# Kernel tuning notes

Measured on AMD Instinct MI355X. Metric: run time of the kernel, lower is better.

## Reference

```python
import jax, jax.numpy as jnp
import numpy as np

H = 768
FF = 3072
NH = 12
DH = H // NH


def setup_inputs() -> dict:
    key = jax.random.key(0)
    ks = jax.random.split(key, 16)
    s = 0.02
    return {
        "latent": jax.random.normal(ks[0], (2, 2048, H), jnp.float32),
        "ln1_w": jnp.ones((H,), jnp.float32),
        "ln1_b": jnp.zeros((H,), jnp.float32),
        "Wq": jax.random.normal(ks[1], (H, H), jnp.float32) * s,
        "bq": jnp.zeros((H,), jnp.float32),
        "Wk": jax.random.normal(ks[2], (H, H), jnp.float32) * s,
        "bk": jnp.zeros((H,), jnp.float32),
        "Wv": jax.random.normal(ks[3], (H, H), jnp.float32) * s,
        "bv": jnp.zeros((H,), jnp.float32),
        "Wo": jax.random.normal(ks[4], (H, H), jnp.float32) * s,
        "bo": jnp.zeros((H,), jnp.float32),
        "ln2_w": jnp.ones((H,), jnp.float32),
        "ln2_b": jnp.zeros((H,), jnp.float32),
        "W1": jax.random.normal(ks[5], (H, FF), jnp.float32) * s,
        "b1": jnp.zeros((FF,), jnp.float32),
        "W2": jax.random.normal(ks[6], (FF, H), jnp.float32) * s,
        "b2": jnp.zeros((H,), jnp.float32),
    }


def _layernorm(x, w, b, eps=1e-6):
    mu = jnp.mean(x, axis=-1, keepdims=True)
    var = jnp.mean(jnp.square(x - mu), axis=-1, keepdims=True)
    return (x - mu) * jax.lax.rsqrt(var + eps) * w + b


def _split_heads(x):  # [B,S,H] -> [B,NH,S,DH]
    B, S, _ = x.shape
    return x.reshape(B, S, NH, DH).transpose(0, 2, 1, 3)


def reference(latent, ln1_w, ln1_b, Wq, bq, Wk, bk, Wv, bv, Wo, bo,
              ln2_w, ln2_b, W1, b1, W2, b2):
    B, S, _ = latent.shape
    # MHSA (dropouts are p=0.0 / eval mode -> identity)
    nx = _layernorm(latent, ln1_w, ln1_b)
    q = _split_heads(nx @ Wq + bq)
    k = _split_heads(nx @ Wk + bk)
    v = _split_heads(nx @ Wv + bv)
    scores = jnp.einsum('bhqd,bhkd->bhqk', q, k) / jnp.sqrt(jnp.float32(DH))
    attn = jax.nn.softmax(scores, axis=-1)
    ctx = jnp.einsum('bhqk,bhkd->bhqd', attn, v)
    ctx = ctx.transpose(0, 2, 1, 3).reshape(B, S, H)
    latent = latent + (ctx @ Wo + bo)
    # FFN (exact erf GELU as in torch nn.GELU default)
    nx = _layernorm(latent, ln2_w, ln2_b)
    h = jax.nn.gelu(nx @ W1 + b1, approximate=False)
    latent = latent + (h @ W2 + b2)
    return latent
```

## Files before the change

kernel.cpp:

```cpp
#include <hip/hip_runtime.h>

#define H 768
#define FF 3072
#define NH 12
#define DH 64
#define SEQ 2048
#define MTOK 4096

typedef __attribute__((ext_vector_type(8))) short short8;
typedef __attribute__((ext_vector_type(4))) float f32x4;
typedef __attribute__((ext_vector_type(2))) unsigned int uint2v;

__device__ __forceinline__ f32x4 mfma16(short8 a, short8 b, f32x4 c) {
  return __builtin_amdgcn_mfma_f32_16x16x32_bf16(a, b, c, 0, 0, 0);
}

__device__ __forceinline__ unsigned short f2bf(float f) {
  union { float f; unsigned int u; } c; c.f = f;
  unsigned int u = c.u;
  u += 0x7fffu + ((u >> 16) & 1u);
  return (unsigned short)(u >> 16);
}
__device__ __forceinline__ float bf2f(unsigned short s) {
  union { unsigned int u; float f; } c; c.u = ((unsigned int)s) << 16;
  return c.f;
}
__device__ __forceinline__ unsigned int pk2bf(float lo, float hi) {
  return (unsigned int)f2bf(lo) | ((unsigned int)f2bf(hi) << 16);
}
__device__ __forceinline__ unsigned int pktrunc(float lo, float hi) {
  union { float f; unsigned int u; } a, b; a.f = hi; b.f = lo;
  return __builtin_amdgcn_perm(a.u, b.u, 0x07060302u);
}

__device__ __forceinline__ void gld16(const unsigned short* g, unsigned short* l) {
  __builtin_amdgcn_global_load_lds(
      (const __attribute__((address_space(1))) void*)g,
      (__attribute__((address_space(3))) void*)l, 16, 0, 0);
}

__global__ __launch_bounds__(256) void prep_kernel(
    const float* __restrict__ Wq, const float* __restrict__ Wk,
    const float* __restrict__ Wv, const float* __restrict__ Wo,
    const float* __restrict__ W1, const float* __restrict__ W2,
    unsigned short* __restrict__ WqkvT, unsigned short* __restrict__ WoT,
    unsigned short* __restrict__ W1T, unsigned short* __restrict__ W2T,
    const float* __restrict__ latent, const float* __restrict__ ln1_w,
    const float* __restrict__ ln1_b, unsigned short* __restrict__ nx) {
  int bid = blockIdx.x;
  int tid = threadIdx.x;
  if (bid >= 6912) {
    int row = bid - 6912;
    const float* xr = latent + (size_t)row * H;
    float v0 = xr[tid], v1 = xr[tid + 256], v2 = xr[tid + 512];
    float s = v0 + v1 + v2;
    float ss = v0 * v0 + v1 * v1 + v2 * v2;
#pragma unroll
    for (int off = 32; off > 0; off >>= 1) {
      s += __shfl_down(s, off);
      ss += __shfl_down(ss, off);
    }
    __shared__ float red[8];
    int wave = tid >> 6, lane = tid & 63;
    if (lane == 0) { red[wave] = s; red[4 + wave] = ss; }
    __syncthreads();
    s = red[0] + red[1] + red[2] + red[3];
    ss = red[4] + red[5] + red[6] + red[7];
    float mu = s * (1.0f / H);
    float var = ss * (1.0f / H) - mu * mu;
    float rs = rsqrtf(var + 1e-6f);
    unsigned short* orow = nx + (size_t)row * H;
    orow[tid]       = f2bf((v0 - mu) * rs * ln1_w[tid]       + ln1_b[tid]);
    orow[tid + 256] = f2bf((v1 - mu) * rs * ln1_w[tid + 256] + ln1_b[tid + 256]);
    orow[tid + 512] = f2bf((v2 - mu) * rs * ln1_w[tid + 512] + ln1_b[tid + 512]);
    return;
  }
  const float* in; unsigned short* out; int K, N, t0;
  if (bid < 1728) {
    K = 768; N = 768;
    if (bid < 576)       { in = Wq; out = WqkvT;                       t0 = bid; }
    else if (bid < 1152) { in = Wk; out = WqkvT + (size_t)768 * 768;   t0 = bid - 576; }
    else                 { in = Wv; out = WqkvT + (size_t)1536 * 768;  t0 = bid - 1152; }
  } else if (bid < 2304) { in = Wo; out = WoT; K = 768;  N = 768;  t0 = bid - 1728; }
  else if (bid < 4608)   { in = W1; out = W1T; K = 768;  N = 3072; t0 = bid - 2304; }
  else                   { in = W2; out = W2T; K = 3072; N = 768;  t0 = bid - 4608; }

  __shared__ float tile[32][33];
  int nb = N >> 5;
  int n0 = (t0 % nb) << 5;
  int k0 = (t0 / nb) << 5;
  int tx = tid & 31, ty = tid >> 5;
#pragma unroll
  for (int yy = 0; yy < 4; ++yy)
    tile[ty + yy * 8][tx] = in[(size_t)(k0 + ty + yy * 8) * N + n0 + tx];
  __syncthreads();
#pragma unroll
  for (int yy = 0; yy < 4; ++yy)
    out[(size_t)(n0 + ty + yy * 8) * K + k0 + tx] = f2bf(tile[tx][ty + yy * 8]);
}

__global__ __launch_bounds__(256) void ln_kernel(const float* __restrict__ x,
                                                 const float* __restrict__ w,
                                                 const float* __restrict__ b,
                                                 unsigned short* __restrict__ out) {
  int row = blockIdx.x;
  int tid = threadIdx.x;
  const float* xr = x + (size_t)row * H;
  float v0 = xr[tid], v1 = xr[tid + 256], v2 = xr[tid + 512];
  float s = v0 + v1 + v2;
  float ss = v0 * v0 + v1 * v1 + v2 * v2;
#pragma unroll
  for (int off = 32; off > 0; off >>= 1) {
    s += __shfl_down(s, off);
    ss += __shfl_down(ss, off);
  }
  __shared__ float red[8];
  int wave = tid >> 6, lane = tid & 63;
  if (lane == 0) { red[wave] = s; red[4 + wave] = ss; }
  __syncthreads();
  s = red[0] + red[1] + red[2] + red[3];
  ss = red[4] + red[5] + red[6] + red[7];
  float mu = s * (1.0f / H);
  float var = ss * (1.0f / H) - mu * mu;
  float rs = rsqrtf(var + 1e-6f);
  unsigned short* orow = out + (size_t)row * H;
  orow[tid]       = f2bf((v0 - mu) * rs * w[tid]       + b[tid]);
  orow[tid + 256] = f2bf((v1 - mu) * rs * w[tid + 256] + b[tid + 256]);
  orow[tid + 512] = f2bf((v2 - mu) * rs * w[tid + 512] + b[tid + 512]);
}

enum { MODE_QKV = 0, MODE_RESID = 1, MODE_GELU = 2 };

template <int MODE>
__global__ __launch_bounds__(256) void gemm128(
    const unsigned short* __restrict__ A,
    const unsigned short* __restrict__ Bt,
    int M, int N, int K,
    const float* __restrict__ bias0,
    const float* __restrict__ bias1,
    const float* __restrict__ bias2,
    unsigned short* __restrict__ out_q,
    unsigned short* __restrict__ out_k,
    unsigned short* __restrict__ out_vT,
    unsigned short* __restrict__ out_bf)
{
  const int mb = M >> 7;
  int m0 = (blockIdx.x % mb) << 7;
  int n0 = (blockIdx.x / mb) << 7;
  int tid = threadIdx.x;
  int wave = tid >> 6, lane = tid & 63;
  int quad = lane >> 4, l16 = lane & 15;
  int wm = (wave & 1) << 6;
  int wn = (wave >> 1) << 6;

  __shared__ __align__(16) unsigned short As[2][128 * 32];
  __shared__ __align__(16) unsigned short Bs[2][128 * 32];

  f32x4 acc[4][4];
#pragma unroll
  for (int i = 0; i < 4; ++i)
#pragma unroll
    for (int j = 0; j < 4; ++j) acc[i][j] = (f32x4){0.f, 0.f, 0.f, 0.f};

  int srow = lane >> 2;
  int scol = (lane & 3) << 3;
  const unsigned short* gA0 = A + (size_t)(m0 + wave * 32 + srow) * K + scol;
  const unsigned short* gA1 = gA0 + (size_t)16 * K;
  const unsigned short* gB0 = Bt + (size_t)(n0 + wave * 32 + srow) * K + scol;
  const unsigned short* gB1 = gB0 + (size_t)16 * K;

  for (int k0 = 0; k0 < K; k0 += 64) {
#pragma unroll
    for (int kc = 0; kc < 2; ++kc) {
      gld16(gA0 + k0 + kc * 32, &As[kc][(wave * 32) * 32]);
      gld16(gA1 + k0 + kc * 32, &As[kc][(wave * 32 + 16) * 32]);
      gld16(gB0 + k0 + kc * 32, &Bs[kc][(wave * 32) * 32]);
      gld16(gB1 + k0 + kc * 32, &Bs[kc][(wave * 32 + 16) * 32]);
    }
    __syncthreads();
#pragma unroll
    for (int kc = 0; kc < 2; ++kc) {
      short8 af[4], bfr[4];
#pragma unroll
      for (int t = 0; t < 4; ++t)
        af[t] = *(const short8*)(&As[kc][(wm + t * 16 + l16) * 32 + quad * 8]);
#pragma unroll
      for (int t = 0; t < 4; ++t)
        bfr[t] = *(const short8*)(&Bs[kc][(wn + t * 16 + l16) * 32 + quad * 8]);
#pragma unroll
      for (int i = 0; i < 4; ++i)
#pragma unroll
        for (int j = 0; j < 4; ++j)
          acc[i][j] = mfma16(af[i], bfr[j], acc[i][j]);
    }
    __syncthreads();
  }

#pragma unroll
  for (int mt = 0; mt < 4; ++mt)
#pragma unroll
    for (int nt = 0; nt < 4; ++nt) {
      f32x4 c = acc[mt][nt];
      int m = m0 + wm + mt * 16 + quad * 4;
      int n = n0 + wn + nt * 16 + l16;
      if (MODE == MODE_QKV) {
        int bb = m >> 11, sIdx = m & 2047;
        if (n < 768) {
          float bs = bias0[n];
          int hh = n >> 6, d = n & 63;
          unsigned short* dst = out_q + (((size_t)(bb * NH + hh)) * SEQ + sIdx) * DH + d;
#pragma unroll
          for (int r = 0; r < 4; ++r) dst[r * DH] = f2bf(c[r] + bs);
        } else if (n < 1536) {
          int nn = n - 768;
          float bs = bias1[nn];
          int hh = nn >> 6, d = nn & 63;
          size_t base = (size_t)(bb * NH + hh) * (SEQ * DH)
                      + (size_t)(sIdx >> 5) * 2048 + ((sIdx >> 4) & 1) * 1024
                      + (d >> 5) * 512 + (sIdx & 15) * 32 + (d & 31);
#pragma unroll
          for (int r = 0; r < 4; ++r) out_k[base + r * 32] = f2bf(c[r] + bs);
        } else {
          int nn = n - 1536;
          float bs = bias2[nn];
          int hh = nn >> 6, d = nn & 63;
          int k5 = sIdx & 31;
          int sa = (k5 & 0x11) | ((k5 & 0x6) << 1) | ((k5 >> 2) & 0x2);
          size_t cb = (size_t)(bb * NH + hh) * (SEQ * DH)
                    + (size_t)(sIdx >> 5) * 2048 + (d >> 4) * 512
                    + (d & 15) * 8 + (size_t)(sa >> 3) * 128;
          *(unsigned int*)(out_vT + cb + (sa & 7))       = pk2bf(c[0] + bs, c[1] + bs);
          *(unsigned int*)(out_vT + cb + ((sa & 7) | 4)) = pk2bf(c[2] + bs, c[3] + bs);
        }
      } else {
        float bs = bias0[n];
        unsigned short* op = out_bf + (size_t)m * N + n;
#pragma unroll
        for (int r = 0; r < 4; ++r) {
          float t = c[r] + bs;
          op[(size_t)r * N] = f2bf(0.5f * t * (1.0f + erff(t * 0.70710678118654752f)));
        }
      }
    }
}

template <int TAG>
__global__ __launch_bounds__(256) void gemm64r(
    const unsigned short* __restrict__ A,
    const unsigned short* __restrict__ Bt,
    int M, int N, int K,
    const float* __restrict__ bias0,
    const float* __restrict__ resid,
    float* __restrict__ out_f)
{
  const int mb = M >> 6;
  int m0 = (blockIdx.x % mb) << 6;
  int n0 = (blockIdx.x / mb) << 6;
  int tid = threadIdx.x;
  int wave = tid >> 6, lane = tid & 63;
  int quad = lane >> 4, l16 = lane & 15;
  int wm = (wave & 1) << 5;
  int wn = (wave >> 1) << 5;

  __shared__ __align__(16) unsigned short As[4][64 * 32];
  __shared__ __align__(16) unsigned short Bs[4][64 * 32];

  f32x4 acc[2][2];
#pragma unroll
  for (int i = 0; i < 2; ++i)
#pragma unroll
    for (int j = 0; j < 2; ++j) acc[i][j] = (f32x4){0.f, 0.f, 0.f, 0.f};

  int srow = lane >> 2;
  int scol = (lane & 3) << 3;
  const unsigned short* gA = A + (size_t)(m0 + wave * 16 + srow) * K + scol;
  const unsigned short* gB = Bt + (size_t)(n0 + wave * 16 + srow) * K + scol;
  unsigned short* lA = &As[0][(wave * 16) * 32];
  unsigned short* lB = &Bs[0][(wave * 16) * 32];
  const int CH = 64 * 32;

  for (int k0 = 0; k0 < K; k0 += 128) {
#pragma unroll
    for (int kc = 0; kc < 4; ++kc) {
      gld16(gA + k0 + kc * 32, lA + kc * CH);
      gld16(gB + k0 + kc * 32, lB + kc * CH);
    }
    __syncthreads();
#pragma unroll
    for (int kc = 0; kc < 4; ++kc) {
      short8 af[2], bfr[2];
#pragma unroll
      for (int t = 0; t < 2; ++t)
        af[t] = *(const short8*)(&As[kc][(wm + t * 16 + l16) * 32 + quad * 8]);
#pragma unroll
      for (int t = 0; t < 2; ++t)
        bfr[t] = *(const short8*)(&Bs[kc][(wn + t * 16 + l16) * 32 + quad * 8]);
#pragma unroll
      for (int i = 0; i < 2; ++i)
#pragma unroll
        for (int j = 0; j < 2; ++j)
          acc[i][j] = mfma16(af[i], bfr[j], acc[i][j]);
    }
    __syncthreads();
  }

#pragma unroll
  for (int mt = 0; mt < 2; ++mt)
#pragma unroll
    for (int nt = 0; nt < 2; ++nt) {
      f32x4 c = acc[mt][nt];
      int m = m0 + wm + mt * 16 + quad * 4;
      int n = n0 + wn + nt * 16 + l16;
      float bs = bias0[n];
      const float* rp = resid + (size_t)m * N + n;
      float* op = out_f + (size_t)m * N + n;
#pragma unroll
      for (int r = 0; r < 4; ++r) op[(size_t)r * N] = rp[(size_t)r * N] + c[r] + bs;
    }
}

__global__ __launch_bounds__(256, 4) void flash_attn_kernel(
    const unsigned short* __restrict__ q,
    const unsigned short* __restrict__ k,
    const unsigned short* __restrict__ vT,
    unsigned short* __restrict__ ctx)
{
  const float CEXP = 0.18033688011112042f;
  int bh = blockIdx.x % 24;
  int qblk = blockIdx.x / 24;
  int b = bh / NH, h = bh % NH;
  int tid = threadIdx.x;
  int wave = tid >> 6, lane = tid & 63;
  int quad = lane >> 4, l16 = lane & 15;
  int qbase = qblk << 5;

  const unsigned short* qp = q + ((size_t)bh * SEQ + qbase) * DH;
  const unsigned short* kbh = k + (size_t)bh * (SEQ * DH);
  const unsigned short* vbh = vT + (size_t)bh * (SEQ * DH);

  short8 qf00 = *(const short8*)(qp + l16 * DH + quad * 8);
  short8 qf01 = *(const short8*)(qp + l16 * DH + 32 + quad * 8);
  short8 qf10 = *(const short8*)(qp + (16 + l16) * DH + quad * 8);
  short8 qf11 = *(const short8*)(qp + (16 + l16) * DH + 32 + quad * 8);

  f32x4 oacc[2][4];
#pragma unroll
  for (int t = 0; t < 2; ++t)
#pragma unroll
    for (int dt = 0; dt < 4; ++dt) oacc[t][dt] = (f32x4){0.f, 0.f, 0.f, 0.f};
  float L[2] = {0.f, 0.f};

  int klin = (l16 * 4 + quad) * 8;
  int vlin = (quad * 16 + l16) * 8;

  int keylo = wave << 9;
  for (int key0 = keylo; key0 < keylo + 512; key0 += 32) {
    int cbase = (key0 >> 5) * 2048;
    short8 ka0 = *(const short8*)(kbh + cbase + klin);
    short8 ka1 = *(const short8*)(kbh + cbase + 512 + klin);
    short8 kb0 = *(const short8*)(kbh + cbase + 1024 + klin);
    short8 kb1 = *(const short8*)(kbh + cbase + 1536 + klin);
    short8 vf0 = *(const short8*)(vbh + cbase + 0 * 512 + vlin);
    short8 vf1 = *(const short8*)(vbh + cbase + 1 * 512 + vlin);
    short8 vf2 = *(const short8*)(vbh + cbase + 2 * 512 + vlin);
    short8 vf3 = *(const short8*)(vbh + cbase + 3 * 512 + vlin);

#pragma unroll
    for (int t = 0; t < 2; ++t) {
      short8 q0 = t ? qf10 : qf00;
      short8 q1 = t ? qf11 : qf01;
      f32x4 s0 = (f32x4){0.f, 0.f, 0.f, 0.f};
      f32x4 s1 = (f32x4){0.f, 0.f, 0.f, 0.f};
      s0 = mfma16(ka0, q0, s0);
      s0 = mfma16(ka1, q1, s0);
      s1 = mfma16(kb0, q0, s1);
      s1 = mfma16(kb1, q1, s1);

      f32x4 p0, p1;
#pragma unroll
      for (int r = 0; r < 4; ++r) {
        p0[r] = __builtin_amdgcn_exp2f(s0[r] * CEXP);
        p1[r] = __builtin_amdgcn_exp2f(s1[r] * CEXP);
      }
      L[t] += (p0[0] + p0[1]) + (p0[2] + p0[3]) + (p1[0] + p1[1]) + (p1[2] + p1[3]);

      unsigned int d00 = pktrunc(p0[0], p0[1]);
      unsigned int d01 = pktrunc(p0[2], p0[3]);
      unsigned int d10 = pktrunc(p1[0], p1[1]);
      unsigned int d11 = pktrunc(p1[2], p1[3]);

      uint2v rA = __builtin_amdgcn_permlane32_swap(d00, d10, false, false);
      uint2v rB = __builtin_amdgcn_permlane32_swap(d01, d11, false, false);
      union { short8 s; unsigned int i[4]; } pf;
      pf.i[0] = rA[0];
      pf.i[1] = rA[1];
      pf.i[2] = rB[0];
      pf.i[3] = rB[1];

      oacc[t][0] = mfma16(vf0, pf.s, oacc[t][0]);
      oacc[t][1] = mfma16(vf1, pf.s, oacc[t][1]);
      oacc[t][2] = mfma16(vf2, pf.s, oacc[t][2]);
      oacc[t][3] = mfma16(vf3, pf.s, oacc[t][3]);
    }
  }

#pragma unroll
  for (int t = 0; t < 2; ++t) {
    L[t] += __shfl_xor(L[t], 16);
    L[t] += __shfl_xor(L[t], 32);
  }

  __shared__ float lbuf[4][2][16];
  __shared__ uint2 obuf[4][2][4][64];

  if (lane < 16) {
    lbuf[wave][0][lane] = L[0];
    lbuf[wave][1][lane] = L[1];
  }
#pragma unroll
  for (int t = 0; t < 2; ++t)
#pragma unroll
    for (int dt = 0; dt < 4; ++dt) {
      uint2 pk;
      pk.x = pk2bf(oacc[t][dt][0], oacc[t][dt][1]);
      pk.y = pk2bf(oacc[t][dt][2], oacc[t][dt][3]);
      obuf[wave][t][dt][lane] = pk;
    }
  __syncthreads();

#pragma unroll
  for (int pp = 0; pp < 2; ++pp) {
    int pi = wave * 2 + pp;
    int t = pi >> 2, dt = pi & 3;
    f32x4 sum = (f32x4){0.f, 0.f, 0.f, 0.f};
#pragma unroll
    for (int w = 0; w < 4; ++w) {
      uint2 pk = obuf[w][t][dt][lane];
      sum[0] += bf2f((unsigned short)(pk.x & 0xffff));
      sum[1] += bf2f((unsigned short)(pk.x >> 16));
      sum[2] += bf2f((unsigned short)(pk.y & 0xffff));
      sum[3] += bf2f((unsigned short)(pk.y >> 16));
    }
    float lstar = lbuf[0][t][l16] + lbuf[1][t][l16] + lbuf[2][t][l16] + lbuf[3][t][l16];
    float rinv = 1.0f / lstar;
    uint2 res;
    res.x = pk2bf(sum[0] * rinv, sum[1] * rinv);
    res.y = pk2bf(sum[2] * rinv, sum[3] * rinv);
    unsigned short* crow = ctx + (size_t)(b * SEQ + qbase + t * 16 + l16) * H
                           + h * DH + dt * 16 + quad * 4;
    *(uint2*)crow = res;
  }
}

extern "C" void kernel_launch(void* const* d_in, const int* in_sizes, int n_in,
                              void* d_out, int out_size, void* d_ws, size_t ws_size,
                              hipStream_t stream) {
  const float* latent = (const float*)d_in[0];
  const float* ln1_w = (const float*)d_in[1];
  const float* ln1_b = (const float*)d_in[2];
  const float* Wq = (const float*)d_in[3];
  const float* bq = (const float*)d_in[4];
  const float* Wk = (const float*)d_in[5];
  const float* bk = (const float*)d_in[6];
  const float* Wv = (const float*)d_in[7];
  const float* bv = (const float*)d_in[8];
  const float* Wo = (const float*)d_in[9];
  const float* bo = (const float*)d_in[10];
  const float* ln2_w = (const float*)d_in[11];
  const float* ln2_b = (const float*)d_in[12];
  const float* W1 = (const float*)d_in[13];
  const float* b1 = (const float*)d_in[14];
  const float* W2 = (const float*)d_in[15];
  const float* b2 = (const float*)d_in[16];
  float* out = (float*)d_out;

  char* ws = (char*)d_ws;
  unsigned short* WqkvT = (unsigned short*)ws; ws += (size_t)2304 * 768 * 2;
  unsigned short* WoT   = (unsigned short*)ws; ws += (size_t)768 * 768 * 2;
  unsigned short* W1T   = (unsigned short*)ws; ws += (size_t)3072 * 768 * 2;
  unsigned short* W2T   = (unsigned short*)ws; ws += (size_t)768 * 3072 * 2;
  unsigned short* nx    = (unsigned short*)ws; ws += (size_t)MTOK * H * 2;
  unsigned short* nx2   = (unsigned short*)ws; ws += (size_t)MTOK * H * 2;
  unsigned short* qb    = (unsigned short*)ws; ws += (size_t)MTOK * H * 2;
  unsigned short* kb    = (unsigned short*)ws; ws += (size_t)MTOK * H * 2;
  unsigned short* vTb   = (unsigned short*)ws; ws += (size_t)MTOK * H * 2;
  unsigned short* ctx   = (unsigned short*)ws; ws += (size_t)MTOK * H * 2;
  unsigned short* hbuf  = (unsigned short*)ws; ws += (size_t)MTOK * FF * 2;
  float* x1             = (float*)ws;          ws += (size_t)MTOK * H * 4;

  prep_kernel<<<6912 + MTOK, 256, 0, stream>>>(
      Wq, Wk, Wv, Wo, W1, W2, WqkvT, WoT, W1T, W2T,
      latent, ln1_w, ln1_b, nx);

  gemm128<MODE_QKV><<<32 * 18, 256, 0, stream>>>(
      nx, WqkvT, MTOK, 2304, 768, bq, bk, bv,
      qb, kb, vTb, nullptr);

  flash_attn_kernel<<<24 * 64, 256, 0, stream>>>(qb, kb, vTb, ctx);

  gemm64r<0><<<64 * 12, 256, 0, stream>>>(
      ctx, WoT, MTOK, 768, 768, bo, latent, x1);

  ln_kernel<<<MTOK, 256, 0, stream>>>(x1, ln2_w, ln2_b, nx2);

  gemm128<MODE_GELU><<<32 * 24, 256, 0, stream>>>(
      nx2, W1T, MTOK, 3072, 768, b1, nullptr, nullptr,
      nullptr, nullptr, nullptr, hbuf);

  gemm64r<1><<<64 * 12, 256, 0, stream>>>(
      hbuf, W2T, MTOK, 768, 3072, b2, x1, out);
}
```

Measured before the change: 270.0 us.

## Store GEMM operands in 16x32 fragment-tiled layout and load MFMA fragments directly

Every producer (LN, weight prep, GELU GEMM output, attention ctx) now writes bf16 data in a blocked 16-row by 32-k tile layout. The GEMMs then load each MFMA fragment straight from global memory with one 16-byte load per lane, with no LDS staging and no barriers. Launch bounds are raised to 4 blocks per SM for occupancy. The cost is that operand reuse across waves now goes through L2/L1 instead of shared memory, so global traffic rises, and there is no explicit prefetch to hide load latency.

```diff
diff --git a/kernel.cpp b/kernel.cpp
--- a/kernel.cpp
+++ b/kernel.cpp
@@ -11,6 +11,7 @@
 typedef __attribute__((ext_vector_type(4))) float f32x4;
 typedef __attribute__((ext_vector_type(2))) unsigned int uint2v;
 
+
 __device__ __forceinline__ f32x4 mfma16(short8 a, short8 b, f32x4 c) {
   return __builtin_amdgcn_mfma_f32_16x16x32_bf16(a, b, c, 0, 0, 0);
 }
@@ -31,12 +32,6 @@
 __device__ __forceinline__ unsigned int pktrunc(float lo, float hi) {
   union { float f; unsigned int u; } a, b; a.f = hi; b.f = lo;
   return __builtin_amdgcn_perm(a.u, b.u, 0x07060302u);
-}
-
-__device__ __forceinline__ void gld16(const unsigned short* g, unsigned short* l) {
-  __builtin_amdgcn_global_load_lds(
-      (const __attribute__((address_space(1))) void*)g,
-      (__attribute__((address_space(3))) void*)l, 16, 0, 0);
 }
 
 __global__ __launch_bounds__(256) void prep_kernel(
@@ -69,10 +64,11 @@
     float mu = s * (1.0f / H);
     float var = ss * (1.0f / H) - mu * mu;
     float rs = rsqrtf(var + 1e-6f);
-    unsigned short* orow = nx + (size_t)row * H;
-    orow[tid]       = f2bf((v0 - mu) * rs * ln1_w[tid]       + ln1_b[tid]);
-    orow[tid + 256] = f2bf((v1 - mu) * rs * ln1_w[tid + 256] + ln1_b[tid + 256]);
-    orow[tid + 512] = f2bf((v2 - mu) * rs * ln1_w[tid + 512] + ln1_b[tid + 512]);
+    unsigned short* orow = nx + (size_t)(row >> 4) * (24 * 512) + (row & 15) * 32;
+    int kb = (tid >> 5) * 512 + (tid & 31);
+    orow[kb]            = f2bf((v0 - mu) * rs * ln1_w[tid]       + ln1_b[tid]);
+    orow[kb + 8 * 512]  = f2bf((v1 - mu) * rs * ln1_w[tid + 256] + ln1_b[tid + 256]);
+    orow[kb + 16 * 512] = f2bf((v2 - mu) * rs * ln1_w[tid + 512] + ln1_b[tid + 512]);
     return;
   }
   const float* in; unsigned short* out; int K, N, t0;
@@ -81,9 +77,10 @@
     if (bid < 576)       { in = Wq; out = WqkvT;                       t0 = bid; }
     else if (bid < 1152) { in = Wk; out = WqkvT + (size_t)768 * 768;   t0 = bid - 576; }
     else                 { in = Wv; out = WqkvT + (size_t)1536 * 768;  t0 = bid - 1152; }
-  } else if (bid < 2304) { in = Wo; out = WoT; K = 768;  N = 768;  t0 = bid - 1728; }
+  } else if (bid < 2304) { in = Wo; out = WoT; K = 768;  N = 3072;  t0 = bid - 1728; }
   else if (bid < 4608)   { in = W1; out = W1T; K = 768;  N = 3072; t0 = bid - 2304; }
   else                   { in = W2; out = W2T; K = 3072; N = 768;  t0 = bid - 4608; }
+  if (bid >= 1728 && bid < 2304) { N = 768; }
 
   __shared__ float tile[32][33];
   int nb = N >> 5;
@@ -94,9 +91,13 @@
   for (int yy = 0; yy < 4; ++yy)
     tile[ty + yy * 8][tx] = in[(size_t)(k0 + ty + yy * 8) * N + n0 + tx];
   __syncthreads();
-#pragma unroll
-  for (int yy = 0; yy < 4; ++yy)
-    out[(size_t)(n0 + ty + yy * 8) * K + k0 + tx] = f2bf(tile[tx][ty + yy * 8]);
+  int KT5 = K >> 5;
+#pragma unroll
+  for (int yy = 0; yy < 4; ++yy) {
+    int n = n0 + ty + yy * 8;
+    out[(size_t)((n >> 4) * KT5 + (k0 >> 5)) * 512 + (n & 15) * 32 + tx]
+        = f2bf(tile[tx][ty + yy * 8]);
+  }
 }
 
 __global__ __launch_bounds__(256) void ln_kernel(const float* __restrict__ x,
@@ -123,16 +124,17 @@
   float mu = s * (1.0f / H);
   float var = ss * (1.0f / H) - mu * mu;
   float rs = rsqrtf(var + 1e-6f);
-  unsigned short* orow = out + (size_t)row * H;
-  orow[tid]       = f2bf((v0 - mu) * rs * w[tid]       + b[tid]);
-  orow[tid + 256] = f2bf((v1 - mu) * rs * w[tid + 256] + b[tid + 256]);
-  orow[tid + 512] = f2bf((v2 - mu) * rs * w[tid + 512] + b[tid + 512]);
+  unsigned short* orow = out + (size_t)(row >> 4) * (24 * 512) + (row & 15) * 32;
+  int kb = (tid >> 5) * 512 + (tid & 31);
+  orow[kb]            = f2bf((v0 - mu) * rs * w[tid]       + b[tid]);
+  orow[kb + 8 * 512]  = f2bf((v1 - mu) * rs * w[tid + 256] + b[tid + 256]);
+  orow[kb + 16 * 512] = f2bf((v2 - mu) * rs * w[tid + 512] + b[tid + 512]);
 }
 
 enum { MODE_QKV = 0, MODE_RESID = 1, MODE_GELU = 2 };
 
 template <int MODE>
-__global__ __launch_bounds__(256) void gemm128(
+__global__ __launch_bounds__(256, 4) void gemm128(
     const unsigned short* __restrict__ A,
     const unsigned short* __restrict__ Bt,
     int M, int N, int K,
@@ -152,9 +154,8 @@
   int quad = lane >> 4, l16 = lane & 15;
   int wm = (wave & 1) << 6;
   int wn = (wave >> 1) << 6;
-
-  __shared__ __align__(16) unsigned short As[2][128 * 32];
-  __shared__ __align__(16) unsigned short Bs[2][128 * 32];
+  int KT = K >> 5;
+  int lof = l16 * 32 + quad * 8;
 
   f32x4 acc[4][4];
 #pragma unroll
@@ -162,38 +163,25 @@
 #pragma unroll
     for (int j = 0; j < 4; ++j) acc[i][j] = (f32x4){0.f, 0.f, 0.f, 0.f};
 
-  int srow = lane >> 2;
-  int scol = (lane & 3) << 3;
-  const unsigned short* gA0 = A + (size_t)(m0 + wave * 32 + srow) * K + scol;
-  const unsigned short* gA1 = gA0 + (size_t)16 * K;
-  const unsigned short* gB0 = Bt + (size_t)(n0 + wave * 32 + srow) * K + scol;
-  const unsigned short* gB1 = gB0 + (size_t)16 * K;
-
-  for (int k0 = 0; k0 < K; k0 += 64) {
-#pragma unroll
-    for (int kc = 0; kc < 2; ++kc) {
-      gld16(gA0 + k0 + kc * 32, &As[kc][(wave * 32) * 32]);
-      gld16(gA1 + k0 + kc * 32, &As[kc][(wave * 32 + 16) * 32]);
-      gld16(gB0 + k0 + kc * 32, &Bs[kc][(wave * 32) * 32]);
-      gld16(gB1 + k0 + kc * 32, &Bs[kc][(wave * 32 + 16) * 32]);
-    }
-    __syncthreads();
-#pragma unroll
-    for (int kc = 0; kc < 2; ++kc) {
-      short8 af[4], bfr[4];
-#pragma unroll
-      for (int t = 0; t < 4; ++t)
-        af[t] = *(const short8*)(&As[kc][(wm + t * 16 + l16) * 32 + quad * 8]);
-#pragma unroll
-      for (int t = 0; t < 4; ++t)
-        bfr[t] = *(const short8*)(&Bs[kc][(wn + t * 16 + l16) * 32 + quad * 8]);
-#pragma unroll
-      for (int i = 0; i < 4; ++i)
-#pragma unroll
-        for (int j = 0; j < 4; ++j)
-          acc[i][j] = mfma16(af[i], bfr[j], acc[i][j]);
-    }
-    __syncthreads();
+  const unsigned short* aP[4];
+  const unsigned short* bP[4];
+#pragma unroll
+  for (int t = 0; t < 4; ++t) {
+    aP[t] = A + (size_t)(((m0 + wm) >> 4) + t) * KT * 512 + lof;
+    bP[t] = Bt + (size_t)(((n0 + wn) >> 4) + t) * KT * 512 + lof;
+  }
+
+  for (int kt = 0; kt < KT; ++kt) {
+    short8 af[4], bfr[4];
+#pragma unroll
+    for (int t = 0; t < 4; ++t) af[t] = *(const short8*)(aP[t] + (size_t)kt * 512);
+#pragma unroll
+    for (int t = 0; t < 4; ++t) bfr[t] = *(const short8*)(bP[t] + (size_t)kt * 512);
+#pragma unroll
+    for (int i = 0; i < 4; ++i)
+#pragma unroll
+      for (int j = 0; j < 4; ++j)
+        acc[i][j] = mfma16(af[i], bfr[j], acc[i][j]);
   }
 
 #pragma unroll
@@ -234,18 +222,20 @@
         }
       } else {
         float bs = bias0[n];
-        unsigned short* op = out_bf + (size_t)m * N + n;
+        int mtile = ((m0 + wm) >> 4) + mt;
+        unsigned short* op = out_bf + (size_t)(mtile * (N >> 5) + (n >> 5)) * 512
+                             + quad * 4 * 32 + (n & 31);
 #pragma unroll
         for (int r = 0; r < 4; ++r) {
           float t = c[r] + bs;
-          op[(size_t)r * N] = f2bf(0.5f * t * (1.0f + erff(t * 0.70710678118654752f)));
+          op[r * 32] = f2bf(0.5f * t * (1.0f + erff(t * 0.70710678118654752f)));
         }
       }
     }
 }
 
 template <int TAG>
-__global__ __launch_bounds__(256) void gemm64r(
+__global__ __launch_bounds__(256, 4) void gemm64r(
     const unsigned short* __restrict__ A,
     const unsigned short* __restrict__ Bt,
     int M, int N, int K,
@@ -261,9 +251,8 @@
   int quad = lane >> 4, l16 = lane & 15;
   int wm = (wave & 1) << 5;
   int wn = (wave >> 1) << 5;
-
-  __shared__ __align__(16) unsigned short As[4][64 * 32];
-  __shared__ __align__(16) unsigned short Bs[4][64 * 32];
+  int KT = K >> 5;
+  int lof = l16 * 32 + quad * 8;
 
   f32x4 acc[2][2];
 #pragma unroll
@@ -271,37 +260,26 @@
 #pragma unroll
     for (int j = 0; j < 2; ++j) acc[i][j] = (f32x4){0.f, 0.f, 0.f, 0.f};
 
-  int srow = lane >> 2;
-  int scol = (lane & 3) << 3;
-  const unsigned short* gA = A + (size_t)(m0 + wave * 16 + srow) * K + scol;
-  const unsigned short* gB = Bt + (size_t)(n0 + wave * 16 + srow) * K + scol;
-  unsigned short* lA = &As[0][(wave * 16) * 32];
-  unsigned short* lB = &Bs[0][(wave * 16) * 32];
-  const int CH = 64 * 32;
-
-  for (int k0 = 0; k0 < K; k0 += 128) {
-#pragma unroll
-    for (int kc = 0; kc < 4; ++kc) {
-      gld16(gA + k0 + kc * 32, lA + kc * CH);
-      gld16(gB + k0 + kc * 32, lB + kc * CH);
-    }
-    __syncthreads();
-#pragma unroll
-    for (int kc = 0; kc < 4; ++kc) {
-      short8 af[2], bfr[2];
-#pragma unroll
-      for (int t = 0; t < 2; ++t)
-        af[t] = *(const short8*)(&As[kc][(wm + t * 16 + l16) * 32 + quad * 8]);
-#pragma unroll
-      for (int t = 0; t < 2; ++t)
-        bfr[t] = *(const short8*)(&Bs[kc][(wn + t * 16 + l16) * 32 + quad * 8]);
-#pragma unroll
-      for (int i = 0; i < 2; ++i)
-#pragma unroll
-        for (int j = 0; j < 2; ++j)
-          acc[i][j] = mfma16(af[i], bfr[j], acc[i][j]);
-    }
-    __syncthreads();
+  const unsigned short* aP[2];
+  const unsigned short* bP[2];
+#pragma unroll
+  for (int t = 0; t < 2; ++t) {
+    aP[t] = A + (size_t)(((m0 + wm) >> 4) + t) * KT * 512 + lof;
+    bP[t] = Bt + (size_t)(((n0 + wn) >> 4) + t) * KT * 512 + lof;
+  }
+
+#pragma unroll 2
+  for (int kt = 0; kt < KT; ++kt) {
+    short8 af[2], bfr[2];
+#pragma unroll
+    for (int t = 0; t < 2; ++t) af[t] = *(const short8*)(aP[t] + (size_t)kt * 512);
+#pragma unroll
+    for (int t = 0; t < 2; ++t) bfr[t] = *(const short8*)(bP[t] + (size_t)kt * 512);
+#pragma unroll
+    for (int i = 0; i < 2; ++i)
+#pragma unroll
+      for (int j = 0; j < 2; ++j)
+        acc[i][j] = mfma16(af[i], bfr[j], acc[i][j]);
   }
 
 #pragma unroll
@@ -446,8 +424,9 @@
     uint2 res;
     res.x = pk2bf(sum[0] * rinv, sum[1] * rinv);
     res.y = pk2bf(sum[2] * rinv, sum[3] * rinv);
-    unsigned short* crow = ctx + (size_t)(b * SEQ + qbase + t * 16 + l16) * H
-                           + h * DH + dt * 16 + quad * 4;
+    unsigned short* crow = ctx
+        + ((size_t)((b * SEQ + qbase + t * 16) >> 4) * 24 + h * 2 + (dt >> 1)) * 512
+        + l16 * 32 + (dt & 1) * 16 + quad * 4;
     *(uint2*)crow = res;
   }
 }
```

Result: slower. 355.9 us (+31.8%).
